# Kernel tuning notes

Measured on AMD Instinct MI355X. Metric: run time of the kernel, lower is better.

## Reference

```python
import jax, jax.numpy as jnp
import numpy as np

B, L, D = 8, 2048, 256


def setup_inputs() -> dict:
    key = jax.random.key(0)
    k1, k2, k3, k4, k5, k6 = jax.random.split(key, 6)
    c1 = jax.random.normal(k1, (B, L, D), dtype=jnp.float32)
    c2 = jax.random.normal(k2, (B, L, D), dtype=jnp.float32)
    c_mask = jnp.zeros((B, L), dtype=bool)  # True = padded position
    # FusionLayer params: linear_f: (4D -> D), linear_g: (4D -> 1)
    s = 1.0 / np.sqrt(4 * D)
    W_f = jax.random.uniform(k3, (4 * D, D), dtype=jnp.float32, minval=-s, maxval=s)
    b_f = jax.random.uniform(k4, (D,), dtype=jnp.float32, minval=-s, maxval=s)
    W_g = jax.random.uniform(k5, (4 * D, 1), dtype=jnp.float32, minval=-s, maxval=s)
    b_g = jax.random.uniform(k6, (1,), dtype=jnp.float32, minval=-s, maxval=s)
    return {"c1": c1, "c2": c2, "c_mask": c_mask, "W_f": W_f, "b_f": b_f,
            "W_g": W_g, "b_g": b_g, "flag": 1}


def reference(c1, c2, c_mask, W_f, b_f, W_g, b_g, flag):
    # flag == 1 -> forward_fuse path
    # AttentionScore default (correlation_func=1): scores[b,i,j] = c2[b,i] . c1[b,j]
    scores = jnp.einsum('bid,bjd->bij', c2, c1)  # [B, L, L]
    neg_inf = jnp.array(-jnp.inf, dtype=scores.dtype)
    diag = jnp.eye(scores.shape[1], dtype=bool)[None]        # [1, L, L]
    scores = jnp.where(diag, neg_inf, scores)                 # mask self-attention diag
    scores = jnp.where(c_mask[:, None, :], neg_inf, scores)   # mask padded keys
    alpha = jax.nn.softmax(scores, axis=2)                    # [B, L, L]
    aug_c2 = jnp.einsum('bij,bjd->bid', alpha, c1)            # [B, L, D]
    # FusionLayer: z = [x, y, x*y, x-y]; out = g*tanh(Wf z) + (1-g)*x
    z = jnp.concatenate([c2, aug_c2, c2 * aug_c2, c2 - aug_c2], axis=2)  # [B, L, 4D]
    gated = jax.nn.sigmoid(z @ W_g + b_g)                     # [B, L, 1]
    fusion = jnp.tanh(z @ W_f + b_f)                          # [B, L, D]
    return gated * fusion + (1.0 - gated) * c2
```

## Files before the change

### kernel.cpp

```cpp
#include <hip/hip_runtime.h>
#include <math.h>

#define BB 8
#define LL 2048
#define DD 256

typedef float  f4_t __attribute__((ext_vector_type(4)));
typedef short  s8_t __attribute__((ext_vector_type(8)));

union S8U { s8_t v; unsigned u[4]; };

__device__ __forceinline__ unsigned bitsf(float x){ union{float f; unsigned u;} c; c.f=x; return c.u; }
__device__ __forceinline__ float fbits(unsigned u){ union{float f; unsigned u;} c; c.u=u; return c.f; }
__device__ __forceinline__ unsigned pkhi(float a, float b){ return (bitsf(a)>>16) | (bitsf(b)&0xffff0000u); }
__device__ __forceinline__ unsigned pkrn(float a, float b){
    unsigned ua = bitsf(a) + 0x8000u, ub = bitsf(b) + 0x8000u;
    return (ua>>16) | (ub&0xffff0000u);
}

__device__ __forceinline__ int vslot(int e){ return ((e>>2)&3)*8 + ((e>>4)<<2) + (e&3); }

__global__ __launch_bounds__(512,1)
void attn_kernel(const float* __restrict__ c1, const float* __restrict__ c2,
                 const unsigned char* __restrict__ cmask,
                 float* __restrict__ o0, float* __restrict__ o1,
                 float* __restrict__ mlp,
                 int klen, int split)
{
    __shared__ short    KhiS[2][32*264];
    __shared__ short    KloS[2][32*264];
    __shared__ unsigned VpS [2][256*20];

    const int tid  = threadIdx.x;
    const int lane = tid & 63;
    const int w    = tid >> 6;
    const int il   = lane & 15;
    const int quad = lane >> 4;
    const int col  = tid & 255;
    const int hr   = (tid >> 8) * 16;

    const int blk  = blockIdx.x;
    const int bb   = blk & 7;
    const int qb   = (blk >> 3) & 15;
    const int half = split ? ((blk >> 7) & 1) : 0;
    const int kb   = half * klen;

    float* ob = half ? o1 : o0;

    const float* c1b = c1 + (size_t)bb * LL * DD;
    const float* c2b = c2 + (size_t)bb * LL * DD;
    const unsigned char* mb = cmask + (size_t)bb * LL;

    const int q0w = qb*128 + w*16;

    s8_t qh[8], ql[8];
    {
        const float* qp = c2b + (size_t)(q0w + il)*DD + quad*8;
#pragma unroll
        for (int kd = 0; kd < 8; ++kd) {
            float4 x0 = *(const float4*)(qp + kd*32);
            float4 x1 = *(const float4*)(qp + kd*32 + 4);
            float e[8] = {x0.x,x0.y,x0.z,x0.w,x1.x,x1.y,x1.z,x1.w};
            S8U h, l;
#pragma unroll
            for (int p2 = 0; p2 < 4; ++p2) {
                float a = e[2*p2], b = e[2*p2+1];
                h.u[p2] = pkhi(a, b);
                float alo = a - fbits(bitsf(a)&0xffff0000u);
                float blo = b - fbits(bitsf(b)&0xffff0000u);
                l.u[p2] = pkhi(alo, blo);
            }
            qh[kd] = h.v; ql[kd] = l.v;
        }
    }

    f4_t o[16];
#pragma unroll
    for (int n = 0; n < 16; ++n) o[n] = (f4_t)0.0f;
    float m_s = -INFINITY;
    float l_s = 0.f;

    const int NT = klen >> 5;
    float g[16];

#define STAGE_WRITE(KH, KL, VP) do { \
    _Pragma("unroll") \
    for (int e_ = 0; e_ < 16; ++e_) { \
        unsigned ub_ = bitsf(g[e_]); \
        (KH)[(hr + e_)*264 + col] = (short)(ub_ >> 16); \
        float lo_ = g[e_] - fbits(ub_ & 0xffff0000u); \
        (KL)[(hr + e_)*264 + col] = (short)(bitsf(lo_) >> 16); \
    } \
    _Pragma("unroll") \
    for (int e_ = 0; e_ < 16; e_ += 2) \
        (VP)[col*20 + (vslot(hr + e_)>>1)] = pkrn(g[e_], g[e_+1]); \
} while (0)

#pragma unroll
    for (int e = 0; e < 16; ++e) g[e] = c1b[(size_t)(kb + hr + e)*DD + col];
    STAGE_WRITE(KhiS[0], KloS[0], VpS[0]);
    __syncthreads();

    int cur = 0;
    for (int kt = 0; kt < NT; ++kt) {
        const int k0 = kt << 5;
        if (kt + 1 < NT) {
#pragma unroll
            for (int e = 0; e < 16; ++e)
                g[e] = c1b[(size_t)(kb + k0 + 32 + hr + e)*DD + col];
        }

        const short*    Khi = KhiS[cur];
        const short*    Klo = KloS[cur];
        const unsigned* Vp  = VpS[cur];

        f4_t acc[2];
        acc[0] = (f4_t)0.0f;
        acc[1] = (f4_t)0.0f;

#pragma unroll
        for (int kd = 0; kd < 8; ++kd) {
            s8_t ah0 = *(const s8_t*)&Khi[(il     )*264 + kd*32 + quad*8];
            s8_t ah1 = *(const s8_t*)&Khi[(16 + il)*264 + kd*32 + quad*8];
            s8_t al0 = *(const s8_t*)&Klo[(il     )*264 + kd*32 + quad*8];
            s8_t al1 = *(const s8_t*)&Klo[(16 + il)*264 + kd*32 + quad*8];
            acc[0] = __builtin_amdgcn_mfma_f32_16x16x32_bf16(ah0, qh[kd], acc[0], 0,0,0);
            acc[1] = __builtin_amdgcn_mfma_f32_16x16x32_bf16(ah1, qh[kd], acc[1], 0,0,0);
            acc[0] = __builtin_amdgcn_mfma_f32_16x16x32_bf16(al0, qh[kd], acc[0], 0,0,0);
            acc[1] = __builtin_amdgcn_mfma_f32_16x16x32_bf16(al1, qh[kd], acc[1], 0,0,0);
            acc[0] = __builtin_amdgcn_mfma_f32_16x16x32_bf16(ah0, ql[kd], acc[0], 0,0,0);
            acc[1] = __builtin_amdgcn_mfma_f32_16x16x32_bf16(ah1, ql[kd], acc[1], 0,0,0);
        }

        unsigned mu[2];
#pragma unroll
        for (int mj = 0; mj < 2; ++mj)
            mu[mj] = *(const unsigned*)(mb + kb + k0 + 16*mj + 4*quad);

        const int ig = q0w + il;
        float tm = -INFINITY;
        f4_t p[2];
#pragma unroll
        for (int mj = 0; mj < 2; ++mj) {
#pragma unroll
            for (int b = 0; b < 4; ++b) {
                int jg = kb + k0 + 16*mj + 4*quad + b;
                float s = acc[mj][b];
                bool dead = (((mu[mj] >> (8*b)) & 0xff) != 0) || (jg == ig);
                s = dead ? -INFINITY : s;
                p[mj][b] = s;
                tm = fmaxf(tm, s);
            }
        }
        tm = fmaxf(tm, __shfl_xor(tm, 16, 64));
        tm = fmaxf(tm, __shfl_xor(tm, 32, 64));
        const bool stable = __all(tm <= m_s);
        const float mn = stable ? m_s : fmaxf(m_s, tm);
        float rs = 0.f;
#pragma unroll
        for (int mj = 0; mj < 2; ++mj) {
#pragma unroll
            for (int b = 0; b < 4; ++b) {
                float pe = __expf(p[mj][b] - mn);
                p[mj][b] = pe;
                rs += pe;
            }
        }
        rs += __shfl_xor(rs, 16, 64);
        rs += __shfl_xor(rs, 32, 64);
        if (!stable) {
            float al = __expf(m_s - mn);
            l_s = l_s*al + rs;
            m_s = mn;
            float am[4];
#pragma unroll
            for (int b = 0; b < 4; ++b) am[b] = __shfl(al, 4*quad + b, 64);
#pragma unroll
            for (int n = 0; n < 16; ++n) {
#pragma unroll
                for (int b = 0; b < 4; ++b) o[n][b] *= am[b];
            }
        } else {
            l_s += rs;
        }

        s8_t ap;
        {
            S8U a;
            a.u[0] = pkrn(p[0][0], p[0][1]);
            a.u[1] = pkrn(p[0][2], p[0][3]);
            a.u[2] = pkrn(p[1][0], p[1][1]);
            a.u[3] = pkrn(p[1][2], p[1][3]);
            ap = a.v;
        }
#pragma unroll
        for (int n = 0; n < 16; ++n) {
            s8_t bv = *(const s8_t*)(Vp + (16*n + il)*20 + quad*4);
            o[n] = __builtin_amdgcn_mfma_f32_16x16x32_bf16(ap, bv, o[n], 0,0,0);
        }

        if (kt + 1 < NT) {
            short*    KhiN = KhiS[cur^1];
            short*    KloN = KloS[cur^1];
            unsigned* VpN  = VpS[cur^1];
            STAGE_WRITE(KhiN, KloN, VpN);
        }
        __syncthreads();
        cur ^= 1;
    }
#undef STAGE_WRITE

    const int rbq = bb*LL + q0w;
    if (split) {
        const int rbase = rbq + 4*quad;
#pragma unroll
        for (int n = 0; n < 16; ++n) {
            const int d = 16*n + il;
#pragma unroll
            for (int b = 0; b < 4; ++b)
                ob[(size_t)(rbase + b)*DD + d] = o[n][b];
        }
        if (lane < 16) {
            int r = rbq + lane;
            *(float2*)(&mlp[((size_t)half*16384 + r)*2]) = make_float2(m_s, l_s);
        }
    } else {
        float invl[4];
#pragma unroll
        for (int b = 0; b < 4; ++b) invl[b] = 1.0f / __shfl(l_s, 4*quad + b, 64);
        const int rbase = rbq + 4*quad;
#pragma unroll
        for (int n = 0; n < 16; ++n) {
            const int d = 16*n + il;
#pragma unroll
            for (int b = 0; b < 4; ++b)
                ob[(size_t)(rbase + b)*DD + d] = o[n][b] * invl[b];
        }
    }
}

__global__ __launch_bounds__(256)
void prep_kernel(const float* __restrict__ Wf, const float* __restrict__ Wg,
                 unsigned* __restrict__ Whi, unsigned* __restrict__ Wlo,
                 float* __restrict__ gw)
{
    if (blockIdx.x == 384) {
#pragma unroll
        for (int i = 0; i < 3; ++i) {
            int kl = threadIdx.x;
            float v = (i == 0) ? (Wg[kl] + Wg[768 + kl])
                    : (i == 1) ? (Wg[256 + kl] - Wg[768 + kl])
                               :  Wg[512 + kl];
            gw[i*256 + kl] = v;
        }
        return;
    }
    int t    = blockIdx.x*256 + threadIdx.x;
    int p    = t & 3;
    int lane = (t >> 2) & 63;
    int nt   = (t >> 8) & 15;
    int g2   = t >> 12;
    int seg  = g2 % 3;
    int kc   = g2 / 3;
    int kl   = kc*32 + (lane >> 4)*8 + 2*p;
    int n    = nt*16 + (lane & 15);
    float v0, v1;
    if (seg == 0) {
        v0 = Wf[(size_t)kl*DD + n]       + Wf[(size_t)(768 + kl)*DD + n];
        v1 = Wf[(size_t)(kl + 1)*DD + n] + Wf[(size_t)(769 + kl)*DD + n];
    } else if (seg == 1) {
        v0 = Wf[(size_t)(256 + kl)*DD + n] - Wf[(size_t)(768 + kl)*DD + n];
        v1 = Wf[(size_t)(257 + kl)*DD + n] - Wf[(size_t)(769 + kl)*DD + n];
    } else {
        v0 = Wf[(size_t)(512 + kl)*DD + n];
        v1 = Wf[(size_t)(513 + kl)*DD + n];
    }
    Whi[t] = pkhi(v0, v1);
    float l0 = v0 - fbits(bitsf(v0) & 0xffff0000u);
    float l1 = v1 - fbits(bitsf(v1) & 0xffff0000u);
    Wlo[t] = pkrn(l0, l1);
}

__global__ __launch_bounds__(512,1)
void fusion_mfma(const float* __restrict__ c2,
                 const float* __restrict__ P0, const float* __restrict__ P1,
                 const float* __restrict__ mlp,
                 const unsigned* __restrict__ Whi, const unsigned* __restrict__ Wlo,
                 const float* __restrict__ gw, const float* __restrict__ bg,
                 const float* __restrict__ bf, float* __restrict__ out, int ns)
{
    __shared__ float gwL[768];
    __shared__ float gv[64];

    const int tid  = threadIdx.x;
    const int lane = tid & 63;
    const int w    = tid >> 6;
    const int il   = lane & 15;
    const int quad = lane >> 4;
    const size_t row0 = (size_t)blockIdx.x * 64;

    const float* c2b = c2 + row0*DD;
    const float* P0b = P0 + row0*DD;
    const float* P1b = P1 + row0*DD;

    for (int i = tid; i < 768; i += 512) gwL[i] = gw[i];

    float ca0[4], ca1[4];
#pragma unroll
    for (int mt = 0; mt < 4; ++mt) { ca0[mt] = 1.f; ca1[mt] = 0.f; }
    if (ns == 2) {
#pragma unroll
        for (int mt = 0; mt < 4; ++mt) {
            const size_t r = row0 + 16*mt + il;
            float m0 = mlp[r*2],             l0 = mlp[r*2 + 1];
            float m1 = mlp[(16384 + r)*2],   l1 = mlp[(16384 + r)*2 + 1];
            float M  = fmaxf(m0, m1);
            float a0 = __expf(m0 - M), a1 = __expf(m1 - M);
            float inv = 1.0f / (a0*l0 + a1*l1);
            ca0[mt] = a0*inv; ca1[mt] = a1*inv;
        }
    }
    __syncthreads();

    f4_t acc[4][2];
#pragma unroll
    for (int mt = 0; mt < 4; ++mt)
#pragma unroll
        for (int nt = 0; nt < 2; ++nt) acc[mt][nt] = (f4_t)0.0f;
    float gp[4] = {0.f, 0.f, 0.f, 0.f};

    for (int kc = 0; kc < 8; ++kc) {
        s8_t za[4], zb[4], zc[4];
        const int c0 = kc*32 + quad*8;
#pragma unroll
        for (int mt = 0; mt < 4; ++mt) {
            const float* pr = c2b + (size_t)(16*mt + il)*DD + c0;
            const float* p0 = P0b + (size_t)(16*mt + il)*DD + c0;
            float4 a0 = *(const float4*)pr, a1 = *(const float4*)(pr + 4);
            f4_t   u0 = *(const f4_t*)p0,   u1 = *(const f4_t*)(p0 + 4);
            if (ns == 2) {
                const float* p1 = P1b + (size_t)(16*mt + il)*DD + c0;
                f4_t v0 = *(const f4_t*)p1, v1 = *(const f4_t*)(p1 + 4);
                u0 = u0*ca0[mt] + v0*ca1[mt];
                u1 = u1*ca0[mt] + v1*ca1[mt];
            }
            float ea[8] = {a0.x,a0.y,a0.z,a0.w,a1.x,a1.y,a1.z,a1.w};
            float eu[8] = {u0[0],u0[1],u0[2],u0[3],u1[0],u1[1],u1[2],u1[3]};
#pragma unroll
            for (int j = 0; j < 8; ++j)
                gp[mt] += ea[j]*gwL[c0+j] + eu[j]*gwL[256+c0+j] + (ea[j]*eu[j])*gwL[512+c0+j];
            S8U A, U, Pd;
#pragma unroll
            for (int p = 0; p < 4; ++p) {
                A.u[p]  = pkrn(ea[2*p], ea[2*p+1]);
                U.u[p]  = pkrn(eu[2*p], eu[2*p+1]);
                Pd.u[p] = pkrn(ea[2*p]*eu[2*p], ea[2*p+1]*eu[2*p+1]);
            }
            za[mt] = A.v; zb[mt] = U.v; zc[mt] = Pd.v;
        }
#pragma unroll
        for (int nt = 0; nt < 2; ++nt) {
            const int ntg = w*2 + nt;
            const size_t f0 = ((size_t)((kc*3 + 0)*16 + ntg)*64 + lane)*4;
            const size_t f1 = ((size_t)((kc*3 + 1)*16 + ntg)*64 + lane)*4;
            const size_t f2 = ((size_t)((kc*3 + 2)*16 + ntg)*64 + lane)*4;
            s8_t w0h = *(const s8_t*)(Whi + f0), w0l = *(const s8_t*)(Wlo + f0);
            s8_t w1h = *(const s8_t*)(Whi + f1), w1l = *(const s8_t*)(Wlo + f1);
            s8_t w2h = *(const s8_t*)(Whi + f2), w2l = *(const s8_t*)(Wlo + f2);
#pragma unroll
            for (int mt = 0; mt < 4; ++mt) {
                acc[mt][nt] = __builtin_amdgcn_mfma_f32_16x16x32_bf16(za[mt], w0h, acc[mt][nt], 0,0,0);
                acc[mt][nt] = __builtin_amdgcn_mfma_f32_16x16x32_bf16(za[mt], w0l, acc[mt][nt], 0,0,0);
                acc[mt][nt] = __builtin_amdgcn_mfma_f32_16x16x32_bf16(zb[mt], w1h, acc[mt][nt], 0,0,0);
                acc[mt][nt] = __builtin_amdgcn_mfma_f32_16x16x32_bf16(zb[mt], w1l, acc[mt][nt], 0,0,0);
                acc[mt][nt] = __builtin_amdgcn_mfma_f32_16x16x32_bf16(zc[mt], w2h, acc[mt][nt], 0,0,0);
                acc[mt][nt] = __builtin_amdgcn_mfma_f32_16x16x32_bf16(zc[mt], w2l, acc[mt][nt], 0,0,0);
            }
        }
    }

#pragma unroll
    for (int mt = 0; mt < 4; ++mt) {
        float gg = gp[mt];
        gg += __shfl_xor(gg, 16, 64);
        gg += __shfl_xor(gg, 32, 64);
        if (w == 0 && quad == 0) gv[16*mt + il] = gg;
    }
    __syncthreads();
    if (tid < 64) gv[tid] = 1.0f / (1.0f + __expf(-(gv[tid] + bg[0])));
    __syncthreads();

#pragma unroll
    for (int nt = 0; nt < 2; ++nt) {
        const int col = w*32 + nt*16 + il;
        const float bfv = bf[col];
#pragma unroll
        for (int mt = 0; mt < 4; ++mt) {
#pragma unroll
            for (int b = 0; b < 4; ++b) {
                const int r = 16*mt + 4*quad + b;
                const float g = gv[r];
                const float cc = c2b[(size_t)r*DD + col];
                out[(row0 + r)*DD + col] = g * tanhf(acc[mt][nt][b] + bfv) + (1.f - g) * cc;
            }
        }
    }
}

extern "C" void kernel_launch(void* const* d_in, const int* in_sizes, int n_in,
                              void* d_out, int out_size, void* d_ws, size_t ws_size,
                              hipStream_t stream)
{
    const float* c1 = (const float*)d_in[0];
    const float* c2 = (const float*)d_in[1];
    const unsigned char* cmask = (const unsigned char*)d_in[2];
    const float* Wf = (const float*)d_in[3];
    const float* bf = (const float*)d_in[4];
    const float* Wg = (const float*)d_in[5];
    const float* bg = (const float*)d_in[6];

    const size_t aug_elems   = (size_t)16384 * 256;
    const size_t frag_elems  = (size_t)98304;

    const size_t ml2_elems = (size_t)2 * 16384 * 2;
    const size_t need2     = (2*aug_elems + ml2_elems + aug_elems) * sizeof(float);

    float* wsf = (float*)d_ws;

    if (ws_size >= need2) {
        float* Op0 = wsf;
        float* Op1 = wsf + aug_elems;
        float* mlp = wsf + 2*aug_elems;
        unsigned* Whi = (unsigned*)(wsf + 2*aug_elems + ml2_elems);
        unsigned* Wlo = Whi + frag_elems;
        float*    gw  = (float*)(Wlo + frag_elems);

        attn_kernel<<<dim3(256), dim3(512), 0, stream>>>(c1, c2, cmask,
                                                         Op0, Op1, mlp, 1024, 1);
        prep_kernel<<<dim3(385), dim3(256), 0, stream>>>(Wf, Wg, Whi, Wlo, gw);
        fusion_mfma<<<dim3(256), dim3(512), 0, stream>>>(c2, Op0, Op1, mlp,
                                                         Whi, Wlo, gw, bg, bf,
                                                         (float*)d_out, 2);
    } else {
        float* aug = wsf;
        unsigned* Whi = (unsigned*)(wsf + aug_elems);
        unsigned* Wlo = Whi + frag_elems;
        float*    gw  = (float*)(Wlo + frag_elems);

        attn_kernel<<<dim3(128), dim3(512), 0, stream>>>(c1, c2, cmask,
                                                         aug, aug, wsf, 2048, 0);
        prep_kernel<<<dim3(385), dim3(256), 0, stream>>>(Wf, Wg, Whi, Wlo, gw);
        fusion_mfma<<<dim3(256), dim3(512), 0, stream>>>(c2, aug, aug, wsf,
                                                         Whi, Wlo, gw, bg, bf,
                                                         (float*)d_out, 1);
    }
}
```

Before: 246.1 us.

## Stage fusion-layer z operands in shared memory with double-buffered prefetch

Previously all 8 waves of a block loaded and converted the same 64x256 c2/P rows into bf16 fragments, repeating that work eight times over. Now each thread loads a single float4 slice, computes the gate partial, packs the bf16 z pieces into double-buffered LDS tiles, and every wave reads its MFMA fragments from LDS. The next chunk's global loads are issued before the MFMAs, which overlaps memory latency with compute. In exchange it adds about 30KB of LDS, a barrier per k-chunk, and a gate reduction through shared memory.

```diff
diff --git a/kernel.cpp b/kernel.cpp
--- a/kernel.cpp
+++ b/kernel.cpp
@@ -289,14 +289,20 @@
                  const float* __restrict__ gw, const float* __restrict__ bg,
                  const float* __restrict__ bf, float* __restrict__ out, int ns)
 {
-    __shared__ float gwL[768];
-    __shared__ float gv[64];
+    __shared__ float    gwL[768];
+    __shared__ unsigned zA[2][64*20];
+    __shared__ unsigned zB[2][64*20];
+    __shared__ unsigned zC[2][64*20];
+    __shared__ float    gpart[64][8];
+    __shared__ float    gv[64];
 
     const int tid  = threadIdx.x;
     const int lane = tid & 63;
     const int w    = tid >> 6;
     const int il   = lane & 15;
     const int quad = lane >> 4;
+    const int srow = tid >> 3;
+    const int scg  = tid & 7;
     const size_t row0 = (size_t)blockIdx.x * 64;
 
     const float* c2b = c2 + row0*DD;
@@ -305,58 +311,65 @@
 
     for (int i = tid; i < 768; i += 512) gwL[i] = gw[i];
 
-    float ca0[4], ca1[4];
-#pragma unroll
-    for (int mt = 0; mt < 4; ++mt) { ca0[mt] = 1.f; ca1[mt] = 0.f; }
+    float ca0 = 1.f, ca1 = 0.f;
     if (ns == 2) {
+        const size_t r = row0 + srow;
+        float m0 = mlp[r*2],             l0 = mlp[r*2 + 1];
+        float m1 = mlp[(16384 + r)*2],   l1 = mlp[(16384 + r)*2 + 1];
+        float M  = fmaxf(m0, m1);
+        float a0 = __expf(m0 - M), a1 = __expf(m1 - M);
+        float inv = 1.0f / (a0*l0 + a1*l1);
+        ca0 = a0*inv; ca1 = a1*inv;
+    }
+    __syncthreads();
+
+    float gatep = 0.f;
+    float4 pr4; f4_t u4;
+
+#define FLOAD(kc_) do { \
+    const int off_ = srow*DD + (kc_)*32 + scg*4; \
+    pr4 = *(const float4*)(c2b + off_); \
+    u4  = *(const f4_t*)(P0b + off_); \
+    if (ns == 2) { \
+        f4_t v4_ = *(const f4_t*)(P1b + off_); \
+        u4 = u4*ca0 + v4_*ca1; \
+    } \
+} while (0)
+
+#define FCONV(buf_, kc_) do { \
+    const int co_ = (kc_)*32 + scg*4; \
+    float ea0_ = pr4.x, ea1_ = pr4.y, ea2_ = pr4.z, ea3_ = pr4.w; \
+    float d0_ = ea0_*u4[0], d1_ = ea1_*u4[1], d2_ = ea2_*u4[2], d3_ = ea3_*u4[3]; \
+    gatep += ea0_*gwL[co_+0] + u4[0]*gwL[256+co_+0] + d0_*gwL[512+co_+0] \
+           + ea1_*gwL[co_+1] + u4[1]*gwL[256+co_+1] + d1_*gwL[512+co_+1] \
+           + ea2_*gwL[co_+2] + u4[2]*gwL[256+co_+2] + d2_*gwL[512+co_+2] \
+           + ea3_*gwL[co_+3] + u4[3]*gwL[256+co_+3] + d3_*gwL[512+co_+3]; \
+    const int zi_ = srow*20 + scg*2; \
+    *(uint2*)&zA[buf_][zi_] = make_uint2(pkrn(ea0_, ea1_), pkrn(ea2_, ea3_)); \
+    *(uint2*)&zB[buf_][zi_] = make_uint2(pkrn(u4[0], u4[1]), pkrn(u4[2], u4[3])); \
+    *(uint2*)&zC[buf_][zi_] = make_uint2(pkrn(d0_, d1_),   pkrn(d2_, d3_)); \
+} while (0)
+
+    f4_t acc[4][2];
+#pragma unroll
+    for (int mt = 0; mt < 4; ++mt)
+#pragma unroll
+        for (int nt = 0; nt < 2; ++nt) acc[mt][nt] = (f4_t)0.0f;
+
+    FLOAD(0); FCONV(0, 0);
+    __syncthreads();
+
+    int cur = 0;
+    for (int kc = 0; kc < 8; ++kc) {
+        if (kc + 1 < 8) FLOAD(kc + 1);
+
+        s8_t fa[4], fb[4], fc[4];
 #pragma unroll
         for (int mt = 0; mt < 4; ++mt) {
-            const size_t r = row0 + 16*mt + il;
-            float m0 = mlp[r*2],             l0 = mlp[r*2 + 1];
-            float m1 = mlp[(16384 + r)*2],   l1 = mlp[(16384 + r)*2 + 1];
-            float M  = fmaxf(m0, m1);
-            float a0 = __expf(m0 - M), a1 = __expf(m1 - M);
-            float inv = 1.0f / (a0*l0 + a1*l1);
-            ca0[mt] = a0*inv; ca1[mt] = a1*inv;
-        }
-    }
-    __syncthreads();
-
-    f4_t acc[4][2];
-#pragma unroll
-    for (int mt = 0; mt < 4; ++mt)
-#pragma unroll
-        for (int nt = 0; nt < 2; ++nt) acc[mt][nt] = (f4_t)0.0f;
-    float gp[4] = {0.f, 0.f, 0.f, 0.f};
-
-    for (int kc = 0; kc < 8; ++kc) {
-        s8_t za[4], zb[4], zc[4];
-        const int c0 = kc*32 + quad*8;
-#pragma unroll
-        for (int mt = 0; mt < 4; ++mt) {
-            const float* pr = c2b + (size_t)(16*mt + il)*DD + c0;
-            const float* p0 = P0b + (size_t)(16*mt + il)*DD + c0;
-            float4 a0 = *(const float4*)pr, a1 = *(const float4*)(pr + 4);
-            f4_t   u0 = *(const f4_t*)p0,   u1 = *(const f4_t*)(p0 + 4);
-            if (ns == 2) {
-                const float* p1 = P1b + (size_t)(16*mt + il)*DD + c0;
-                f4_t v0 = *(const f4_t*)p1, v1 = *(const f4_t*)(p1 + 4);
-                u0 = u0*ca0[mt] + v0*ca1[mt];
-                u1 = u1*ca0[mt] + v1*ca1[mt];
-            }
-            float ea[8] = {a0.x,a0.y,a0.z,a0.w,a1.x,a1.y,a1.z,a1.w};
-            float eu[8] = {u0[0],u0[1],u0[2],u0[3],u1[0],u1[1],u1[2],u1[3]};
-#pragma unroll
-            for (int j = 0; j < 8; ++j)
-                gp[mt] += ea[j]*gwL[c0+j] + eu[j]*gwL[256+c0+j] + (ea[j]*eu[j])*gwL[512+c0+j];
-            S8U A, U, Pd;
-#pragma unroll
-            for (int p = 0; p < 4; ++p) {
-                A.u[p]  = pkrn(ea[2*p], ea[2*p+1]);
-                U.u[p]  = pkrn(eu[2*p], eu[2*p+1]);
-                Pd.u[p] = pkrn(ea[2*p]*eu[2*p], ea[2*p+1]*eu[2*p+1]);
-            }
-            za[mt] = A.v; zb[mt] = U.v; zc[mt] = Pd.v;
+            const int fi = (16*mt + il)*20 + quad*4;
+            fa[mt] = *(const s8_t*)&zA[cur][fi];
+            fb[mt] = *(const s8_t*)&zB[cur][fi];
+            fc[mt] = *(const s8_t*)&zC[cur][fi];
         }
 #pragma unroll
         for (int nt = 0; nt < 2; ++nt) {
@@ -369,25 +382,30 @@
             s8_t w2h = *(const s8_t*)(Whi + f2), w2l = *(const s8_t*)(Wlo + f2);
 #pragma unroll
             for (int mt = 0; mt < 4; ++mt) {
-                acc[mt][nt] = __builtin_amdgcn_mfma_f32_16x16x32_bf16(za[mt], w0h, acc[mt][nt], 0,0,0);
-                acc[mt][nt] = __builtin_amdgcn_mfma_f32_16x16x32_bf16(za[mt], w0l, acc[mt][nt], 0,0,0);
-                acc[mt][nt] = __builtin_amdgcn_mfma_f32_16x16x32_bf16(zb[mt], w1h, acc[mt][nt], 0,0,0);
-                acc[mt][nt] = __builtin_amdgcn_mfma_f32_16x16x32_bf16(zb[mt], w1l, acc[mt][nt], 0,0,0);
-                acc[mt][nt] = __builtin_amdgcn_mfma_f32_16x16x32_bf16(zc[mt], w2h, acc[mt][nt], 0,0,0);
-                acc[mt][nt] = __builtin_amdgcn_mfma_f32_16x16x32_bf16(zc[mt], w2l, acc[mt][nt], 0,0,0);
-            }
-        }
-    }
-
-#pragma unroll
-    for (int mt = 0; mt < 4; ++mt) {
-        float gg = gp[mt];
-        gg += __shfl_xor(gg, 16, 64);
-        gg += __shfl_xor(gg, 32, 64);
-        if (w == 0 && quad == 0) gv[16*mt + il] = gg;
-    }
+                acc[mt][nt] = __builtin_amdgcn_mfma_f32_16x16x32_bf16(fa[mt], w0h, acc[mt][nt], 0,0,0);
+                acc[mt][nt] = __builtin_amdgcn_mfma_f32_16x16x32_bf16(fa[mt], w0l, acc[mt][nt], 0,0,0);
+                acc[mt][nt] = __builtin_amdgcn_mfma_f32_16x16x32_bf16(fb[mt], w1h, acc[mt][nt], 0,0,0);
+                acc[mt][nt] = __builtin_amdgcn_mfma_f32_16x16x32_bf16(fb[mt], w1l, acc[mt][nt], 0,0,0);
+                acc[mt][nt] = __builtin_amdgcn_mfma_f32_16x16x32_bf16(fc[mt], w2h, acc[mt][nt], 0,0,0);
+                acc[mt][nt] = __builtin_amdgcn_mfma_f32_16x16x32_bf16(fc[mt], w2l, acc[mt][nt], 0,0,0);
+            }
+        }
+
+        if (kc + 1 < 8) FCONV(cur ^ 1, kc + 1);
+        __syncthreads();
+        cur ^= 1;
+    }
+#undef FLOAD
+#undef FCONV
+
+    gpart[srow][scg] = gatep;
     __syncthreads();
-    if (tid < 64) gv[tid] = 1.0f / (1.0f + __expf(-(gv[tid] + bg[0])));
+    if (tid < 64) {
+        float s = 0.f;
+#pragma unroll
+        for (int cg = 0; cg < 8; ++cg) s += gpart[tid][cg];
+        gv[tid] = 1.0f / (1.0f + __expf(-(s + bg[0])));
+    }
     __syncthreads();
 
 #pragma unroll
```

Result: faster. 222.4 us (-9.7%).
